# Kernel tuning notes

Measured on AMD Instinct MI355X. Metric: run time of the kernel, lower is better.

## Reference

```python
import math
import jax, jax.numpy as jnp
import numpy as np

N_KINDS = 8
D_MODEL = 256
B_FEAT = 24  # Fourier bands; MLP input dim is 2*B_FEAT
SIGMA = 8.0


def setup_inputs() -> dict:
    key = jax.random.key(0)
    ks = jax.random.split(key, 8)
    N, S = 32, 2048
    values = jax.random.normal(ks[0], (N, S, 1), dtype=jnp.float32)
    kinds = jax.random.randint(ks[1], (N, S), 0, N_KINDS, dtype=jnp.int32)
    # Frozen Fourier projection matrix (torch: randn(in_dim, B) * sigma, requires_grad=False)
    Bmat = jax.random.normal(ks[2], (1, B_FEAT), dtype=jnp.float32) * SIGMA
    # Kind embedding table
    kind_emb = jax.random.normal(ks[3], (N_KINDS, D_MODEL), dtype=jnp.float32) * 0.02
    # Per-kind two-layer MLP params
    W1 = jax.random.normal(ks[4], (N_KINDS, 2 * B_FEAT, D_MODEL), dtype=jnp.float32) / math.sqrt(2 * B_FEAT)
    b1 = jnp.zeros((N_KINDS, D_MODEL), dtype=jnp.float32)
    W2 = jax.random.normal(ks[5], (N_KINDS, D_MODEL, D_MODEL), dtype=jnp.float32) / math.sqrt(D_MODEL)
    b2 = jnp.zeros((N_KINDS, D_MODEL), dtype=jnp.float32)
    return {"values": values, "kinds": kinds, "Bmat": Bmat,
            "kind_emb": kind_emb, "W1": W1, "b1": b1, "W2": W2, "b2": b2}


def reference(values, kinds, Bmat, kind_emb, W1, b1, W2, b2):
    N, S, _ = values.shape
    T = N * S
    d = kind_emb.shape[-1]
    # Fourier features: [T, 2B]
    y = (2.0 * math.pi) * values.reshape(T, 1) @ Bmat  # [T, B]
    ff = jnp.concatenate([jnp.sin(y), jnp.cos(y)], axis=-1)  # [T, 2B]
    kinds_flat = kinds.reshape(T)
    out = jnp.zeros((T, d), dtype=values.dtype)
    # kinds partition the tokens, so masked combine == the torch scatter-assign
    for k in range(kind_emb.shape[0]):
        h = jax.nn.gelu(ff @ W1[k] + b1[k], approximate=False)  # torch GELU is exact erf
        o = h @ W2[k] + b2[k]  # [T, d]
        out = jnp.where((kinds_flat == k)[:, None], o, out)
    return out.reshape(N, S, d) + kind_emb[kinds]
```

## Files before the change

kernel.cpp:

```cpp
#include <hip/hip_runtime.h>
#include <hip/hip_bf16.h>
#include <math.h>


#define NK 8
#define DM 256
#define TMAX 65536
#define NBLK 256
#define W1PK 16384
#define W2PK 65536
#define LDSTRIDE 262

typedef __attribute__((ext_vector_type(8))) short   s16x8;
typedef __attribute__((ext_vector_type(8))) __bf16  bf16x8;
typedef __attribute__((ext_vector_type(4))) float   f32x4;
typedef __attribute__((ext_vector_type(2))) float   f32x2;
typedef __attribute__((ext_vector_type(4))) int     i32x4;

__device__ int   g_counts[NK];
__device__ __align__(16) int g_blkcnt[NBLK][NK];
__device__ int   g_bucket[(size_t)NK * TMAX];
__device__ __align__(16) short g_W1p[(size_t)NK * W1PK];
__device__ __align__(16) short g_W2p[(size_t)NK * W2PK];

static __device__ __forceinline__ short f2bf(float f) {
    __hip_bfloat16 h = __float2bfloat16(f);
    return __builtin_bit_cast(short, h);
}

static __device__ __forceinline__ short pkbf(float f) {
    unsigned u = __builtin_bit_cast(unsigned, f);
    return (short)((u + 0x8000u) >> 16);
}

static __device__ __forceinline__ f32x4 mfma16(s16x8 a, s16x8 b, f32x4 c) {
    return __builtin_amdgcn_mfma_f32_16x16x32_bf16(
        __builtin_bit_cast(bf16x8, a), __builtin_bit_cast(bf16x8, b), c, 0, 0, 0);
}

static __device__ __forceinline__ float gelu_fast(float x) {
    float t1 = x * x;
    float m  = fmaf(0.0713548162726f, t1, 1.59576912161f);
    float z  = m * x;
    float e  = __expf(-z);
    return x * __frcp_rn(1.0f + e);
}

__global__ __launch_bounds__(256) void prep_kernel(const float* __restrict__ W1,
                                                   const float* __restrict__ W2,
                                                   const int* __restrict__ kinds, int T) {
    __shared__ float ld[32 * LDSTRIDE];
    __shared__ int wcnt[4][NK];
    const int tid = threadIdx.x;
    const int bid = blockIdx.x;
    if (bid < 80) {
        const int isW1 = (bid >= 64);
        int kind, kt;
        if (isW1) { kind = (bid - 64) >> 1; kt = (bid - 64) & 1; }
        else      { kind = bid >> 3;        kt = bid & 7; }
        #pragma unroll
        for (int i = 0; i < 8; ++i) {
            int f = tid + i * 256;
            int row = f >> 6, col = (f & 63) * 4;
            int kk = kt * 32 + row;
            f32x4 v = (f32x4){0.f, 0.f, 0.f, 0.f};
            if (isW1) {
                if (kk < 48) v = *(const f32x4*)(W1 + ((size_t)kind * 48 + kk) * DM + col);
            } else {
                v = *(const f32x4*)(W2 + ((size_t)kind * DM + kk) * DM + col);
            }
            float* dst = &ld[row * LDSTRIDE + col];
            *(f32x2*)dst       = (f32x2){v[0], v[1]};
            *(f32x2*)(dst + 2) = (f32x2){v[2], v[3]};
        }
        __syncthreads();
        short* outp = isW1 ? (g_W1p + (size_t)kind * W1PK) : (g_W2p + (size_t)kind * W2PK);
        #pragma unroll
        for (int i = 0; i < 4; ++i) {
            int g = tid + i * 256;
            int ntile = g >> 6, l = g & 63;
            int kk0 = (l >> 4) * 8, n = ntile * 16 + (l & 15);
            s16x8 v;
            #pragma unroll
            for (int j = 0; j < 8; ++j) v[j] = f2bf(ld[(kk0 + j) * LDSTRIDE + n]);
            *(s16x8*)(outp + ((size_t)(kt * 16 + ntile) * 64 + l) * 8) = v;
        }
    } else {
        const int b = bid - 80;
        const int wave = tid >> 6, lane = tid & 63;
        int t = b * 256 + tid;
        int k = (t < T) ? kinds[t] : -1;
        #pragma unroll
        for (int kk = 0; kk < NK; ++kk) {
            unsigned long long m = __ballot(k == kk);
            if (lane == 0) wcnt[wave][kk] = __popcll(m);
        }
        __syncthreads();
        if (tid < NK) {
            int s = 0;
            #pragma unroll
            for (int w = 0; w < 4; ++w) s += wcnt[w][tid];
            g_blkcnt[b][tid] = s;
        }
    }
}

__global__ __launch_bounds__(256) void scatter_kernel(const int* __restrict__ kinds, int T) {
    __shared__ int cnt_s[NBLK * NK];
    __shared__ int chunksum[32][NK];
    __shared__ int chunkpref[32][NK];
    __shared__ int wcnt[4][NK];
    __shared__ int base_s[NK];
    const int tid = threadIdx.x, wave = tid >> 6, lane = tid & 63;
    const int b = blockIdx.x;
    {
        const i32x4* src = (const i32x4*)&g_blkcnt[0][0];
        i32x4* dst = (i32x4*)cnt_s;
        dst[tid]       = src[tid];
        dst[tid + 256] = src[tid + 256];
    }
    int t = b * 256 + tid;
    int k = (t < T) ? kinds[t] : -1;
    int rank = 0;
    #pragma unroll
    for (int kk = 0; kk < NK; ++kk) {
        unsigned long long m = __ballot(k == kk);
        if (lane == 0) wcnt[wave][kk] = __popcll(m);
        if (k == kk) rank = __popcll(m & ((1ull << lane) - 1ull));
    }
    __syncthreads();
    {
        int kk = tid & 7, ch = tid >> 3;
        int s = 0;
        #pragma unroll
        for (int i = 0; i < 8; ++i) s += cnt_s[(ch * 8 + i) * NK + kk];
        chunksum[ch][kk] = s;
    }
    __syncthreads();
    if (tid < NK) {
        int s = 0;
        #pragma unroll
        for (int ch = 0; ch < 32; ++ch) { chunkpref[ch][tid] = s; s += chunksum[ch][tid]; }
        if (b == 0) g_counts[tid] = s;
        int ch = b >> 3;
        int s2 = chunkpref[ch][tid];
        for (int bb = ch * 8; bb < b; ++bb) s2 += cnt_s[bb * NK + tid];
        base_s[tid] = s2;
        int ws = 0;
        #pragma unroll
        for (int w = 0; w < 4; ++w) { int c = wcnt[w][tid]; wcnt[w][tid] = ws; ws += c; }
    }
    __syncthreads();
    if (k >= 0)
        g_bucket[(size_t)k * T + base_s[k] + wcnt[wave][k] + rank] = t;
}

__global__ __launch_bounds__(256, 4) void fproj_gemm(
    const float* __restrict__ values, const float* __restrict__ Bmat,
    const float* __restrict__ kind_emb, const float* __restrict__ b1,
    const float* __restrict__ b2, float* __restrict__ out, int T)
{
    int cnts[NK];
    #pragma unroll
    for (int i = 0; i < NK; ++i) cnts[i] = g_counts[i];
    const int bid = blockIdx.x;
    int k = -1, m0 = 0, cum = 0, cnt = 0;
    #pragma unroll
    for (int kk = 0; kk < NK; ++kk) {
        int tk = (cnts[kk] + 31) >> 5;
        if (k < 0 && bid < cum + tk) { k = kk; m0 = (bid - cum) * 32; cnt = cnts[kk]; }
        cum += tk;
    }
    if (k < 0) return;
    const int valid = min(32, cnt - m0);
    const int* buck = g_bucket + (size_t)k * T + m0;

    __shared__ short Hpack[8192];

    const int tid  = threadIdx.x;
    const int wave = tid >> 6;
    const int lane = tid & 63;
    const int quad = lane >> 4;
    const int cl   = lane & 15;

    float vm[2];
    vm[0] = (cl < valid)      ? values[buck[cl]]      : 0.0f;
    vm[1] = (16 + cl < valid) ? values[buck[16 + cl]] : 0.0f;
    s16x8 a0[2], a1[2];
    #pragma unroll
    for (int mt = 0; mt < 2; ++mt) {
        float v = vm[mt];
        #pragma unroll
        for (int j = 0; j < 8; ++j) {
            int b0 = (quad == 3) ? j : quad * 8 + j;
            float r0 = __builtin_amdgcn_fractf(v * Bmat[b0]);
            float s0 = __builtin_amdgcn_sinf(r0);
            float c0 = __builtin_amdgcn_cosf(r0);
            a0[mt][j] = pkbf((quad == 3) ? c0 : s0);
            int b1i = min(8 * (quad + 1) + j, 23);
            float r1 = __builtin_amdgcn_fractf(v * Bmat[b1i]);
            float c1 = __builtin_amdgcn_cosf(r1);
            a1[mt][j] = pkbf((quad < 2) ? c1 : 0.0f);
        }
    }

    f32x4 acc[2][4];
    #pragma unroll
    for (int mt = 0; mt < 2; ++mt)
        #pragma unroll
        for (int nt = 0; nt < 4; ++nt) acc[mt][nt] = (f32x4){0.f, 0.f, 0.f, 0.f};
    const s16x8* B1p = (const s16x8*)(g_W1p + (size_t)k * W1PK);
    #pragma unroll
    for (int kt = 0; kt < 2; ++kt) {
        s16x8 bf[4];
        #pragma unroll
        for (int nt = 0; nt < 4; ++nt) bf[nt] = B1p[(kt * 16 + wave * 4 + nt) * 64 + lane];
        #pragma unroll
        for (int mt = 0; mt < 2; ++mt) {
            s16x8 a = kt ? a1[mt] : a0[mt];
            #pragma unroll
            for (int nt = 0; nt < 4; ++nt) acc[mt][nt] = mfma16(a, bf[nt], acc[mt][nt]);
        }
    }

    #pragma unroll
    for (int nt = 0; nt < 4; ++nt) {
        int c = wave * 64 + nt * 16 + cl;
        float bias = b1[k * DM + c];
        int kt2 = c >> 5, q2 = (c >> 3) & 3, j2 = c & 7;
        #pragma unroll
        for (int mt = 0; mt < 2; ++mt) {
            short* hp = Hpack + (kt2 * 2 + mt) * 512 + (q2 << 4) * 8 + j2;
            #pragma unroll
            for (int r = 0; r < 4; ++r) {
                int m = quad * 4 + r;
                float h = gelu_fast(acc[mt][nt][r] + bias);
                hp[m * 8] = pkbf(h);
            }
        }
    }
    __syncthreads();

    float addc[4];
    #pragma unroll
    for (int nt = 0; nt < 4; ++nt) {
        int c = wave * 64 + nt * 16 + cl;
        addc[nt] = b2[k * DM + c] + kind_emb[k * DM + c];
    }

    f32x4 acc2[2][4];
    #pragma unroll
    for (int mt = 0; mt < 2; ++mt)
        #pragma unroll
        for (int nt = 0; nt < 4; ++nt) acc2[mt][nt] = (f32x4){0.f, 0.f, 0.f, 0.f};
    const s16x8* Hp  = (const s16x8*)Hpack;
    const s16x8* B2p = (const s16x8*)(g_W2p + (size_t)k * W2PK);
    #pragma unroll
    for (int kt = 0; kt < 8; ++kt) {
        s16x8 am[2];
        #pragma unroll
        for (int mt = 0; mt < 2; ++mt) am[mt] = Hp[(kt * 2 + mt) * 64 + lane];
        s16x8 bf[4];
        #pragma unroll
        for (int nt = 0; nt < 4; ++nt) bf[nt] = B2p[(kt * 16 + wave * 4 + nt) * 64 + lane];
        #pragma unroll
        for (int mt = 0; mt < 2; ++mt)
            #pragma unroll
            for (int nt = 0; nt < 4; ++nt) acc2[mt][nt] = mfma16(am[mt], bf[nt], acc2[mt][nt]);
    }

    #pragma unroll
    for (int mt = 0; mt < 2; ++mt)
        #pragma unroll
        for (int r = 0; r < 4; ++r) {
            int row = mt * 16 + quad * 4 + r;
            if (row < valid) {
                size_t ro = (size_t)buck[row] * DM;
                #pragma unroll
                for (int nt = 0; nt < 4; ++nt) {
                    int c = wave * 64 + nt * 16 + cl;
                    __builtin_nontemporal_store(acc2[mt][nt][r] + addc[nt], out + ro + c);
                }
            }
        }
}

extern "C" void kernel_launch(void* const* d_in, const int* in_sizes, int n_in,
                              void* d_out, int out_size, void* d_ws, size_t ws_size,
                              hipStream_t stream) {
    const float* values   = (const float*)d_in[0];
    const int*   kinds    = (const int*)  d_in[1];
    const float* Bmat     = (const float*)d_in[2];
    const float* kind_emb = (const float*)d_in[3];
    const float* W1       = (const float*)d_in[4];
    const float* b1       = (const float*)d_in[5];
    const float* W2       = (const float*)d_in[6];
    const float* b2       = (const float*)d_in[7];
    float* out = (float*)d_out;
    const int T = in_sizes[0];

    prep_kernel<<<dim3(80 + NBLK), dim3(256), 0, stream>>>(W1, W2, kinds, T);
    scatter_kernel<<<dim3(NBLK), dim3(256), 0, stream>>>(kinds, T);
    fproj_gemm<<<dim3(T / 32 + NK), dim3(256), 0, stream>>>(values, Bmat, kind_emb,
                                                            b1, b2, out, T);
}
```

Measured before the change: 118.9 us.

## Replace two-pass bucket scan with atomic bucketing and enlarge GEMM tiles

```diff
diff --git a/kernel.cpp b/kernel.cpp
--- a/kernel.cpp
+++ b/kernel.cpp
@@ -15,10 +15,8 @@
 typedef __attribute__((ext_vector_type(8))) __bf16  bf16x8;
 typedef __attribute__((ext_vector_type(4))) float   f32x4;
 typedef __attribute__((ext_vector_type(2))) float   f32x2;
-typedef __attribute__((ext_vector_type(4))) int     i32x4;
-
-__device__ int   g_counts[NK];
-__device__ __align__(16) int g_blkcnt[NBLK][NK];
+
+__device__ __align__(16) int g_counts[NK * 32];
 __device__ int   g_bucket[(size_t)NK * TMAX];
 __device__ __align__(16) short g_W1p[(size_t)NK * W1PK];
 __device__ __align__(16) short g_W2p[(size_t)NK * W2PK];
@@ -49,11 +47,10 @@
 __global__ __launch_bounds__(256) void prep_kernel(const float* __restrict__ W1,
                                                    const float* __restrict__ W2,
                                                    const int* __restrict__ kinds, int T) {
-    __shared__ float ld[32 * LDSTRIDE];
-    __shared__ int wcnt[4][NK];
     const int tid = threadIdx.x;
     const int bid = blockIdx.x;
     if (bid < 80) {
+        __shared__ float ld[32 * LDSTRIDE];
         const int isW1 = (bid >= 64);
         int kind, kt;
         if (isW1) { kind = (bid - 64) >> 1; kt = (bid - 64) & 1; }
@@ -86,151 +83,116 @@
             *(s16x8*)(outp + ((size_t)(kt * 16 + ntile) * 64 + l) * 8) = v;
         }
     } else {
+        __shared__ int wcnt[4][NK];
+        __shared__ int base_s[NK];
         const int b = bid - 80;
         const int wave = tid >> 6, lane = tid & 63;
         int t = b * 256 + tid;
         int k = (t < T) ? kinds[t] : -1;
+        int rank = 0;
         #pragma unroll
         for (int kk = 0; kk < NK; ++kk) {
             unsigned long long m = __ballot(k == kk);
             if (lane == 0) wcnt[wave][kk] = __popcll(m);
+            if (k == kk) rank = __popcll(m & ((1ull << lane) - 1ull));
         }
         __syncthreads();
         if (tid < NK) {
-            int s = 0;
-            #pragma unroll
-            for (int w = 0; w < 4; ++w) s += wcnt[w][tid];
-            g_blkcnt[b][tid] = s;
-        }
-    }
-}
-
-__global__ __launch_bounds__(256) void scatter_kernel(const int* __restrict__ kinds, int T) {
-    __shared__ int cnt_s[NBLK * NK];
-    __shared__ int chunksum[32][NK];
-    __shared__ int chunkpref[32][NK];
-    __shared__ int wcnt[4][NK];
-    __shared__ int base_s[NK];
-    const int tid = threadIdx.x, wave = tid >> 6, lane = tid & 63;
-    const int b = blockIdx.x;
-    {
-        const i32x4* src = (const i32x4*)&g_blkcnt[0][0];
-        i32x4* dst = (i32x4*)cnt_s;
-        dst[tid]       = src[tid];
-        dst[tid + 256] = src[tid + 256];
-    }
-    int t = b * 256 + tid;
-    int k = (t < T) ? kinds[t] : -1;
-    int rank = 0;
-    #pragma unroll
-    for (int kk = 0; kk < NK; ++kk) {
-        unsigned long long m = __ballot(k == kk);
-        if (lane == 0) wcnt[wave][kk] = __popcll(m);
-        if (k == kk) rank = __popcll(m & ((1ull << lane) - 1ull));
-    }
-    __syncthreads();
-    {
-        int kk = tid & 7, ch = tid >> 3;
-        int s = 0;
-        #pragma unroll
-        for (int i = 0; i < 8; ++i) s += cnt_s[(ch * 8 + i) * NK + kk];
-        chunksum[ch][kk] = s;
-    }
-    __syncthreads();
-    if (tid < NK) {
-        int s = 0;
-        #pragma unroll
-        for (int ch = 0; ch < 32; ++ch) { chunkpref[ch][tid] = s; s += chunksum[ch][tid]; }
-        if (b == 0) g_counts[tid] = s;
-        int ch = b >> 3;
-        int s2 = chunkpref[ch][tid];
-        for (int bb = ch * 8; bb < b; ++bb) s2 += cnt_s[bb * NK + tid];
-        base_s[tid] = s2;
-        int ws = 0;
-        #pragma unroll
-        for (int w = 0; w < 4; ++w) { int c = wcnt[w][tid]; wcnt[w][tid] = ws; ws += c; }
-    }
-    __syncthreads();
-    if (k >= 0)
-        g_bucket[(size_t)k * T + base_s[k] + wcnt[wave][k] + rank] = t;
-}
-
-__global__ __launch_bounds__(256, 4) void fproj_gemm(
+            int ws = 0;
+            #pragma unroll
+            for (int w = 0; w < 4; ++w) { int c = wcnt[w][tid]; wcnt[w][tid] = ws; ws += c; }
+            base_s[tid] = atomicAdd(&g_counts[tid * 32], ws);
+        }
+        __syncthreads();
+        if (k >= 0)
+            g_bucket[(size_t)k * T + base_s[k] + wcnt[wave][k] + rank] = t;
+    }
+}
+
+__global__ __launch_bounds__(512, 4) void fproj_gemm(
     const float* __restrict__ values, const float* __restrict__ Bmat,
     const float* __restrict__ kind_emb, const float* __restrict__ b1,
     const float* __restrict__ b2, float* __restrict__ out, int T)
 {
     int cnts[NK];
     #pragma unroll
-    for (int i = 0; i < NK; ++i) cnts[i] = g_counts[i];
+    for (int i = 0; i < NK; ++i) cnts[i] = g_counts[i * 32];
     const int bid = blockIdx.x;
     int k = -1, m0 = 0, cum = 0, cnt = 0;
     #pragma unroll
     for (int kk = 0; kk < NK; ++kk) {
-        int tk = (cnts[kk] + 31) >> 5;
-        if (k < 0 && bid < cum + tk) { k = kk; m0 = (bid - cum) * 32; cnt = cnts[kk]; }
+        int tk = (cnts[kk] + 63) >> 6;
+        if (k < 0 && bid < cum + tk) { k = kk; m0 = (bid - cum) * 64; cnt = cnts[kk]; }
         cum += tk;
     }
     if (k < 0) return;
-    const int valid = min(32, cnt - m0);
+    const int valid = min(64, cnt - m0);
     const int* buck = g_bucket + (size_t)k * T + m0;
 
-    __shared__ short Hpack[8192];
+    __shared__ short Hpack[16384];
 
     const int tid  = threadIdx.x;
-    const int wave = tid >> 6;
+    const int wv   = tid >> 6;
     const int lane = tid & 63;
     const int quad = lane >> 4;
     const int cl   = lane & 15;
 
-    float vm[2];
-    vm[0] = (cl < valid)      ? values[buck[cl]]      : 0.0f;
-    vm[1] = (16 + cl < valid) ? values[buck[16 + cl]] : 0.0f;
-    s16x8 a0[2], a1[2];
-    #pragma unroll
-    for (int mt = 0; mt < 2; ++mt) {
+    float vm[4];
+    #pragma unroll
+    for (int mt = 0; mt < 4; ++mt) {
+        int row = mt * 16 + cl;
+        vm[mt] = (row < valid) ? values[buck[row]] : 0.0f;
+    }
+    float bb0[8], bb1[8];
+    const float add0 = (quad == 3) ? 0.25f : 0.0f;
+    #pragma unroll
+    for (int j = 0; j < 8; ++j) {
+        int b0 = (quad == 3) ? j : quad * 8 + j;
+        bb0[j] = Bmat[b0];
+        int b1i = min(8 * (quad + 1) + j, 23);
+        bb1[j] = Bmat[b1i];
+    }
+    s16x8 a0[4], a1[4];
+    #pragma unroll
+    for (int mt = 0; mt < 4; ++mt) {
         float v = vm[mt];
         #pragma unroll
         for (int j = 0; j < 8; ++j) {
-            int b0 = (quad == 3) ? j : quad * 8 + j;
-            float r0 = __builtin_amdgcn_fractf(v * Bmat[b0]);
-            float s0 = __builtin_amdgcn_sinf(r0);
-            float c0 = __builtin_amdgcn_cosf(r0);
-            a0[mt][j] = pkbf((quad == 3) ? c0 : s0);
-            int b1i = min(8 * (quad + 1) + j, 23);
-            float r1 = __builtin_amdgcn_fractf(v * Bmat[b1i]);
-            float c1 = __builtin_amdgcn_cosf(r1);
+            float r0 = __builtin_amdgcn_fractf(fmaf(v, bb0[j], add0));
+            a0[mt][j] = pkbf(__builtin_amdgcn_sinf(r0));
+            float r1 = __builtin_amdgcn_fractf(fmaf(v, bb1[j], 0.25f));
+            float c1 = __builtin_amdgcn_sinf(r1);
             a1[mt][j] = pkbf((quad < 2) ? c1 : 0.0f);
         }
     }
 
-    f32x4 acc[2][4];
-    #pragma unroll
-    for (int mt = 0; mt < 2; ++mt)
-        #pragma unroll
-        for (int nt = 0; nt < 4; ++nt) acc[mt][nt] = (f32x4){0.f, 0.f, 0.f, 0.f};
+    f32x4 acc[4][2];
+    #pragma unroll
+    for (int mt = 0; mt < 4; ++mt)
+        #pragma unroll
+        for (int nt = 0; nt < 2; ++nt) acc[mt][nt] = (f32x4){0.f, 0.f, 0.f, 0.f};
     const s16x8* B1p = (const s16x8*)(g_W1p + (size_t)k * W1PK);
     #pragma unroll
     for (int kt = 0; kt < 2; ++kt) {
-        s16x8 bf[4];
-        #pragma unroll
-        for (int nt = 0; nt < 4; ++nt) bf[nt] = B1p[(kt * 16 + wave * 4 + nt) * 64 + lane];
-        #pragma unroll
-        for (int mt = 0; mt < 2; ++mt) {
+        s16x8 bf[2];
+        #pragma unroll
+        for (int nt = 0; nt < 2; ++nt) bf[nt] = B1p[(kt * 16 + wv * 2 + nt) * 64 + lane];
+        #pragma unroll
+        for (int mt = 0; mt < 4; ++mt) {
             s16x8 a = kt ? a1[mt] : a0[mt];
             #pragma unroll
-            for (int nt = 0; nt < 4; ++nt) acc[mt][nt] = mfma16(a, bf[nt], acc[mt][nt]);
-        }
-    }
-
-    #pragma unroll
-    for (int nt = 0; nt < 4; ++nt) {
-        int c = wave * 64 + nt * 16 + cl;
+            for (int nt = 0; nt < 2; ++nt) acc[mt][nt] = mfma16(a, bf[nt], acc[mt][nt]);
+        }
+    }
+
+    #pragma unroll
+    for (int nt = 0; nt < 2; ++nt) {
+        int c = wv * 32 + nt * 16 + cl;
         float bias = b1[k * DM + c];
         int kt2 = c >> 5, q2 = (c >> 3) & 3, j2 = c & 7;
         #pragma unroll
-        for (int mt = 0; mt < 2; ++mt) {
-            short* hp = Hpack + (kt2 * 2 + mt) * 512 + (q2 << 4) * 8 + j2;
+        for (int mt = 0; mt < 4; ++mt) {
+            short* hp = Hpack + (kt2 * 4 + mt) * 512 + q2 * 128 + j2;
             #pragma unroll
             for (int r = 0; r < 4; ++r) {
                 int m = quad * 4 + r;
@@ -241,44 +203,44 @@
     }
     __syncthreads();
 
-    float addc[4];
-    #pragma unroll
-    for (int nt = 0; nt < 4; ++nt) {
-        int c = wave * 64 + nt * 16 + cl;
+    float addc[2];
+    #pragma unroll
+    for (int nt = 0; nt < 2; ++nt) {
+        int c = wv * 32 + nt * 16 + cl;
         addc[nt] = b2[k * DM + c] + kind_emb[k * DM + c];
     }
 
-    f32x4 acc2[2][4];
-    #pragma unroll
-    for (int mt = 0; mt < 2; ++mt)
-        #pragma unroll
-        for (int nt = 0; nt < 4; ++nt) acc2[mt][nt] = (f32x4){0.f, 0.f, 0.f, 0.f};
+    f32x4 acc2[4][2];
+    #pragma unroll
+    for (int mt = 0; mt < 4; ++mt)
+        #pragma unroll
+        for (int nt = 0; nt < 2; ++nt) acc2[mt][nt] = (f32x4){0.f, 0.f, 0.f, 0.f};
     const s16x8* Hp  = (const s16x8*)Hpack;
     const s16x8* B2p = (const s16x8*)(g_W2p + (size_t)k * W2PK);
     #pragma unroll
     for (int kt = 0; kt < 8; ++kt) {
-        s16x8 am[2];
-        #pragma unroll
-        for (int mt = 0; mt < 2; ++mt) am[mt] = Hp[(kt * 2 + mt) * 64 + lane];
-        s16x8 bf[4];
-        #pragma unroll
-        for (int nt = 0; nt < 4; ++nt) bf[nt] = B2p[(kt * 16 + wave * 4 + nt) * 64 + lane];
-        #pragma unroll
-        for (int mt = 0; mt < 2; ++mt)
-            #pragma unroll
-            for (int nt = 0; nt < 4; ++nt) acc2[mt][nt] = mfma16(am[mt], bf[nt], acc2[mt][nt]);
-    }
-
-    #pragma unroll
-    for (int mt = 0; mt < 2; ++mt)
+        s16x8 am[4];
+        #pragma unroll
+        for (int mt = 0; mt < 4; ++mt) am[mt] = Hp[(kt * 4 + mt) * 64 + lane];
+        s16x8 bf[2];
+        #pragma unroll
+        for (int nt = 0; nt < 2; ++nt) bf[nt] = B2p[(kt * 16 + wv * 2 + nt) * 64 + lane];
+        #pragma unroll
+        for (int mt = 0; mt < 4; ++mt)
+            #pragma unroll
+            for (int nt = 0; nt < 2; ++nt) acc2[mt][nt] = mfma16(am[mt], bf[nt], acc2[mt][nt]);
+    }
+
+    #pragma unroll
+    for (int mt = 0; mt < 4; ++mt)
         #pragma unroll
         for (int r = 0; r < 4; ++r) {
             int row = mt * 16 + quad * 4 + r;
             if (row < valid) {
                 size_t ro = (size_t)buck[row] * DM;
                 #pragma unroll
-                for (int nt = 0; nt < 4; ++nt) {
-                    int c = wave * 64 + nt * 16 + cl;
+                for (int nt = 0; nt < 2; ++nt) {
+                    int c = wv * 32 + nt * 16 + cl;
                     __builtin_nontemporal_store(acc2[mt][nt][r] + addc[nt], out + ro + c);
                 }
             }
@@ -299,8 +261,11 @@
     float* out = (float*)d_out;
     const int T = in_sizes[0];
 
+    static void* cnt_addr = nullptr;
+    if (!cnt_addr) (void)hipGetSymbolAddress(&cnt_addr, HIP_SYMBOL(g_counts));
+    hipMemsetAsync(cnt_addr, 0, sizeof(int) * NK * 32, stream);
+
     prep_kernel<<<dim3(80 + NBLK), dim3(256), 0, stream>>>(W1, W2, kinds, T);
-    scatter_kernel<<<dim3(NBLK), dim3(256), 0, stream>>>(kinds, T);
-    fproj_gemm<<<dim3(T / 32 + NK), dim3(256), 0, stream>>>(values, Bmat, kind_emb,
+    fproj_gemm<<<dim3(T / 64 + NK), dim3(512), 0, stream>>>(values, Bmat, kind_emb,
                                                             b1, b2, out, T);
 }
```

Result: no change. 120.9 us (+1.7%).
